# Optimization experiments

Measured on AMD Instinct MI355X. Metric: run time of the kernel, lower is better.

The kernel has to match this reference:

```python
import jax, jax.numpy as jnp
import numpy as np

N, E, D_IN, D_OUT = 50000, 800000, 128, 64


def setup_inputs() -> dict:
    key = jax.random.key(0)
    ks = jax.random.split(key, 8)
    s = 1.0 / np.sqrt(D_IN)
    return {
        "x": jax.random.normal(ks[0], (N, D_IN), jnp.float32),
        "edge_index": jax.random.randint(ks[1], (2, E), 0, N),
        "edge_weight": jax.random.uniform(ks[2], (E,), jnp.float32),
        "init_w": jax.random.normal(ks[3], (D_IN, D_IN), jnp.float32) * s,
        "gru_w_ih": jax.random.normal(ks[4], (3 * D_IN, D_IN), jnp.float32) * s,
        "gru_w_hh": jax.random.normal(ks[5], (3 * D_IN, D_IN), jnp.float32) * s,
        "gru_b_ih": jnp.zeros((3 * D_IN,), jnp.float32),
        "gru_b_hh": jnp.zeros((3 * D_IN,), jnp.float32),
        "lin_w": jax.random.normal(ks[6], (D_OUT, D_IN), jnp.float32) * s,
        "lin_b": jnp.zeros((D_OUT,), jnp.float32),
    }


def _gru_step(x, h, w_ih, w_hh, b_ih, b_hh):
    # torch GRU gate order: r, z, n
    gi = x @ w_ih.T + b_ih
    gh = h @ w_hh.T + b_hh
    i_r, i_z, i_n = jnp.split(gi, 3, axis=-1)
    h_r, h_z, h_n = jnp.split(gh, 3, axis=-1)
    r = jax.nn.sigmoid(i_r + h_r)
    z = jax.nn.sigmoid(i_z + h_z)
    n = jnp.tanh(i_n + r * h_n)
    return (1.0 - z) * n + z * h


def reference(x, edge_index, edge_weight, init_w, gru_w_ih, gru_w_hh, gru_b_ih, gru_b_hh, lin_w, lin_b):
    n_nodes = x.shape[0]
    # EvolveGCNO: evolve W via one GRU step, W is both input and hidden (rows = GRU batch)
    W = _gru_step(init_w, init_w, gru_w_ih, gru_w_hh, gru_b_ih, gru_b_hh)  # [D_IN, D_IN]

    # gcn_norm with self-loops (fill value 1.0)
    loop = jnp.arange(n_nodes)
    row = jnp.concatenate([edge_index[0], loop])  # source j
    col = jnp.concatenate([edge_index[1], loop])  # target i
    w = jnp.concatenate([edge_weight, jnp.ones((n_nodes,), x.dtype)])
    deg = jax.ops.segment_sum(w, col, num_segments=n_nodes)
    dis = jnp.where(deg > 0, jax.lax.rsqrt(jnp.maximum(deg, 1e-12)), 0.0)
    norm = dis[row] * w * dis[col]  # [E+N]

    xw = x @ W  # [N, D_IN]
    h = jax.ops.segment_sum(norm[:, None] * xw[row], col, num_segments=n_nodes)
    h = jax.nn.relu(h)
    return h @ lin_w.T + lin_b  # [N, D_OUT]
```

## Files before the change

### kernel.cpp

```cpp
#include <hip/hip_runtime.h>
#include <hip/hip_fp16.h>
#include <math.h>

#define NN 50000
#define NE 800000
#define D  128
#define D3 384
#define DO 64

typedef _Float16 f16x2 __attribute__((ext_vector_type(2)));

__device__ __forceinline__ float dot2acc(unsigned int h2bits, unsigned int wbits,
                                         float acc) {
#if __has_builtin(__builtin_amdgcn_fdot2)
  return __builtin_amdgcn_fdot2(__builtin_bit_cast(f16x2, h2bits),
                                __builtin_bit_cast(f16x2, wbits), acc, false);
#else
  float2 hf = __half22float2(__builtin_bit_cast(__half2, h2bits));
  float2 wf = __half22float2(__builtin_bit_cast(__half2, wbits));
  return acc + hf.x * wf.x + hf.y * wf.y;
#endif
}

__device__ __forceinline__ unsigned int pk_f16(float a, float b) {
#if __has_builtin(__builtin_amdgcn_cvt_pkrtz)
  return __builtin_bit_cast(unsigned int, __builtin_amdgcn_cvt_pkrtz(a, b));
#else
  return __builtin_bit_cast(unsigned int, __floats2half2_rn(a, b));
#endif
}

__global__ __launch_bounds__(256) void setup_kernel(
    const float* __restrict__ init_w, const float* __restrict__ w_ih,
    const float* __restrict__ w_hh, const float* __restrict__ b_ih,
    const float* __restrict__ b_hh, __half* __restrict__ Wh,
    unsigned long long* __restrict__ packed, int* __restrict__ total) {
  if (blockIdx.x >= 64) {
    int i = (blockIdx.x - 64) * 256 + threadIdx.x;
    if (i < NN) packed[i] = (1ULL << 32);
    if (i == 0) *total = 0;
    return;
  }
  int idx = blockIdx.x * 256 + threadIdx.x;
  int b = idx >> 7;
  int j = idx & 127;
  const float* xr = init_w + b * D;
  const float* wr_i = w_ih + j * D;
  const float* wz_i = w_ih + (D + j) * D;
  const float* wn_i = w_ih + (2 * D + j) * D;
  const float* wr_h = w_hh + j * D;
  const float* wz_h = w_hh + (D + j) * D;
  const float* wn_h = w_hh + (2 * D + j) * D;
  float ir = 0.f, iz = 0.f, in_ = 0.f, hr = 0.f, hz = 0.f, hn = 0.f;
#pragma unroll 4
  for (int k = 0; k < D; ++k) {
    float xv = xr[k];
    ir += xv * wr_i[k];
    iz += xv * wz_i[k];
    in_ += xv * wn_i[k];
    hr += xv * wr_h[k];
    hz += xv * wz_h[k];
    hn += xv * wn_h[k];
  }
  ir += b_ih[j];       hr += b_hh[j];
  iz += b_ih[D + j];   hz += b_hh[D + j];
  in_ += b_ih[2 * D + j]; hn += b_hh[2 * D + j];
  float r = 1.f / (1.f + expf(-(ir + hr)));
  float z = 1.f / (1.f + expf(-(iz + hz)));
  float n = tanhf(in_ + r * hn);
  Wh[idx] = (__half)((1.f - z) * n + z * init_w[idx]);
}

__global__ __launch_bounds__(256) void count_deg_kernel(const int* __restrict__ col,
                                                        const float* __restrict__ ew,
                                                        unsigned long long* __restrict__ packed,
                                                        int* __restrict__ rank) {
  int e = blockIdx.x * 256 + threadIdx.x;
  if (e < NE) {
    int c = __builtin_nontemporal_load(&col[e]);
    float w = __builtin_nontemporal_load(&ew[e]);
    unsigned long long add = (1ULL << 40) | (unsigned long long)(w * 4294967296.0f);
    unsigned long long old = atomicAdd(&packed[c], add);
    __builtin_nontemporal_store((int)(old >> 40), &rank[e]);
  }
}

__global__ __launch_bounds__(256) void dis_scan_kernel(
    const unsigned long long* __restrict__ packed, float* __restrict__ dis,
    int* __restrict__ cnt, int* __restrict__ start, int* __restrict__ total) {
  int i = blockIdx.x * 256 + threadIdx.x;
  int lane = threadIdx.x & 63;
  int c = 0;
  float d = 1.0f;
  if (i < NN) {
    unsigned long long p = packed[i];
    c = (int)(p >> 40);
    d = (float)(p & ((1ULL << 40) - 1)) * 0x1p-32f;
  }
  int cp = (c + 3) & ~3;
  int pre = cp;
#pragma unroll
  for (int off = 1; off < 64; off <<= 1) {
    int t = __shfl_up(pre, off, 64);
    if (lane >= off) pre += t;
  }
  int excl = pre - cp;
  int wtot = __shfl(pre, 63, 64);
  int base = 0;
  if (lane == 63) base = atomicAdd(total, wtot);
  base = __shfl(base, 63, 64);
  if (i < NN) {
    start[i] = base + excl;
    cnt[i] = c;
    dis[i] = rsqrtf(fmaxf(d, 1e-12f));
  }
}

__global__ __launch_bounds__(256) void bucket_kernel(
    const int* __restrict__ row, const int* __restrict__ col,
    const float* __restrict__ ew, const int* __restrict__ rank,
    const int* __restrict__ start, unsigned int* __restrict__ epack) {
  int e = blockIdx.x * 256 + threadIdx.x;
  if (e >= NE) return;
  int j = __builtin_nontemporal_load(&row[e]);
  int c = __builtin_nontemporal_load(&col[e]);
  float w = __builtin_nontemporal_load(&ew[e]);
  int rk = __builtin_nontemporal_load(&rank[e]);
  unsigned short wb = __builtin_bit_cast(unsigned short, (_Float16)w);
  int slot = start[c] + rk;
  __builtin_nontemporal_store((unsigned int)j | ((unsigned int)wb << 16),
                              &epack[slot]);
}

__global__ __launch_bounds__(256) void xw_kernel(const float* __restrict__ x,
                                                 const __half* __restrict__ Wh,
                                                 const float* __restrict__ dis,
                                                 __half* __restrict__ ywh) {
  __shared__ unsigned int U[64 * 128];
  {
    const unsigned short* Wu = (const unsigned short*)Wh;
    for (int i = threadIdx.x; i < 64 * 128; i += 256) {
      int kp = i >> 7, c = i & 127;
      unsigned int lo = Wu[(2 * kp) * D + c];
      unsigned int hi = Wu[(2 * kp + 1) * D + c];
      U[i] = lo | (hi << 16);
    }
  }
  __syncthreads();
  const int t = threadIdx.x;
  const int rr = t >> 4;
  const int ci = t & 15;
  const uint4* U4 = (const uint4*)U;
  for (int base = blockIdx.x * 32; base < NN; base += gridDim.x * 32) {
    float acc[2][8];
#pragma unroll
    for (int q = 0; q < 2; ++q)
#pragma unroll
      for (int j = 0; j < 8; ++j) acc[q][j] = 0.f;
    const int r0 = base + rr;
    const int r1 = r0 + 16;
    const bool v0 = r0 < NN, v1 = r1 < NN;
    const float* xp0 = x + (long)r0 * D;
    const float* xp1 = x + (long)r1 * D;
#pragma unroll 2
    for (int k0 = 0; k0 < D; k0 += 4) {
      float4 xa = v0 ? *(const float4*)(xp0 + k0) : make_float4(0.f, 0.f, 0.f, 0.f);
      float4 xb = v1 ? *(const float4*)(xp1 + k0) : make_float4(0.f, 0.f, 0.f, 0.f);
      unsigned int xa0 = pk_f16(xa.x, xa.y), xa1 = pk_f16(xa.z, xa.w);
      unsigned int xb0 = pk_f16(xb.x, xb.y), xb1 = pk_f16(xb.z, xb.w);
      int kp = k0 >> 1;
      uint4 wA = U4[kp * 32 + 2 * ci];
      uint4 wB = U4[kp * 32 + 2 * ci + 1];
      uint4 wC = U4[(kp + 1) * 32 + 2 * ci];
      uint4 wD = U4[(kp + 1) * 32 + 2 * ci + 1];
      acc[0][0] = dot2acc(xa0, wA.x, acc[0][0]);
      acc[0][1] = dot2acc(xa0, wA.y, acc[0][1]);
      acc[0][2] = dot2acc(xa0, wA.z, acc[0][2]);
      acc[0][3] = dot2acc(xa0, wA.w, acc[0][3]);
      acc[0][4] = dot2acc(xa0, wB.x, acc[0][4]);
      acc[0][5] = dot2acc(xa0, wB.y, acc[0][5]);
      acc[0][6] = dot2acc(xa0, wB.z, acc[0][6]);
      acc[0][7] = dot2acc(xa0, wB.w, acc[0][7]);
      acc[1][0] = dot2acc(xb0, wA.x, acc[1][0]);
      acc[1][1] = dot2acc(xb0, wA.y, acc[1][1]);
      acc[1][2] = dot2acc(xb0, wA.z, acc[1][2]);
      acc[1][3] = dot2acc(xb0, wA.w, acc[1][3]);
      acc[1][4] = dot2acc(xb0, wB.x, acc[1][4]);
      acc[1][5] = dot2acc(xb0, wB.y, acc[1][5]);
      acc[1][6] = dot2acc(xb0, wB.z, acc[1][6]);
      acc[1][7] = dot2acc(xb0, wB.w, acc[1][7]);
      acc[0][0] = dot2acc(xa1, wC.x, acc[0][0]);
      acc[0][1] = dot2acc(xa1, wC.y, acc[0][1]);
      acc[0][2] = dot2acc(xa1, wC.z, acc[0][2]);
      acc[0][3] = dot2acc(xa1, wC.w, acc[0][3]);
      acc[0][4] = dot2acc(xa1, wD.x, acc[0][4]);
      acc[0][5] = dot2acc(xa1, wD.y, acc[0][5]);
      acc[0][6] = dot2acc(xa1, wD.z, acc[0][6]);
      acc[0][7] = dot2acc(xa1, wD.w, acc[0][7]);
      acc[1][0] = dot2acc(xb1, wC.x, acc[1][0]);
      acc[1][1] = dot2acc(xb1, wC.y, acc[1][1]);
      acc[1][2] = dot2acc(xb1, wC.z, acc[1][2]);
      acc[1][3] = dot2acc(xb1, wC.w, acc[1][3]);
      acc[1][4] = dot2acc(xb1, wD.x, acc[1][4]);
      acc[1][5] = dot2acc(xb1, wD.y, acc[1][5]);
      acc[1][6] = dot2acc(xb1, wD.z, acc[1][6]);
      acc[1][7] = dot2acc(xb1, wD.w, acc[1][7]);
    }
#pragma unroll
    for (int q = 0; q < 2; ++q) {
      int r = r0 + q * 16;
      if (r < NN) {
        float ds = dis[r];
        unsigned int pk[4];
#pragma unroll
        for (int j = 0; j < 4; ++j)
          pk[j] = __builtin_bit_cast(unsigned int,
                                     __floats2half2_rn(ds * acc[q][2 * j],
                                                       ds * acc[q][2 * j + 1]));
        *(uint4*)(ywh + (long)r * D + ci * 8) = *(uint4*)pk;
      }
    }
  }
}

__global__ __launch_bounds__(256) void gather_out_kernel(
    const int* __restrict__ start, const int* __restrict__ cnt,
    const unsigned int* __restrict__ epack, const float* __restrict__ dis,
    const __half* __restrict__ ywh, const float* __restrict__ lin_w,
    const float* __restrict__ lin_b, float* __restrict__ out) {
  __shared__ unsigned int LTh[64 * 64];
  __shared__ unsigned int hb[4][2][64];
  for (int idx = threadIdx.x; idx < 64 * 64; idx += 256) {
    int kk = idx >> 6, o = idx & 63;
    __half2 w2 = __floats2half2_rn(lin_w[o * D + 2 * kk], lin_w[o * D + 2 * kk + 1]);
    LTh[idx] = __builtin_bit_cast(unsigned int, w2);
  }
  __syncthreads();
  const int wv = threadIdx.x >> 6;
  const int lane = threadIdx.x & 63;
  const float bias = lin_b[lane];
  const __half2* __restrict__ yw2 = (const __half2*)ywh;
  int gw = blockIdx.x * 4 + wv;
  int nw = gridDim.x * 4;
  for (int i = gw; i < NN; i += 2 * nw) {
    const int iB = i + nw;
    const bool hasB = iB < NN;
    float2 svA = __half22float2(yw2[(long)i * 64 + lane]);
    float aA0 = svA.x, aA1 = svA.y;
    float aB0 = 0.f, aB1 = 0.f;
    int sA = start[i], seA = sA + cnt[i];
    int sB = 0, seB = 0;
    if (hasB) {
      float2 svB = __half22float2(yw2[(long)iB * 64 + lane]);
      aB0 = svB.x;
      aB1 = svB.y;
      sB = start[iB];
      seB = sB + cnt[iB];
    }
    while (sA + 4 <= seA && sB + 4 <= seB) {
      uint4 pA = *(const uint4*)(epack + sA);
      uint4 pB = *(const uint4*)(epack + sB);
      __half2 vA0 = yw2[(long)(pA.x & 0xffff) * 64 + lane];
      __half2 vA1 = yw2[(long)(pA.y & 0xffff) * 64 + lane];
      __half2 vA2 = yw2[(long)(pA.z & 0xffff) * 64 + lane];
      __half2 vA3 = yw2[(long)(pA.w & 0xffff) * 64 + lane];
      __half2 vB0 = yw2[(long)(pB.x & 0xffff) * 64 + lane];
      __half2 vB1 = yw2[(long)(pB.y & 0xffff) * 64 + lane];
      __half2 vB2 = yw2[(long)(pB.z & 0xffff) * 64 + lane];
      __half2 vB3 = yw2[(long)(pB.w & 0xffff) * 64 + lane];
      _Float16 wA0 = __builtin_bit_cast(_Float16, (unsigned short)(pA.x >> 16));
      _Float16 wA1 = __builtin_bit_cast(_Float16, (unsigned short)(pA.y >> 16));
      _Float16 wA2 = __builtin_bit_cast(_Float16, (unsigned short)(pA.z >> 16));
      _Float16 wA3 = __builtin_bit_cast(_Float16, (unsigned short)(pA.w >> 16));
      _Float16 wB0 = __builtin_bit_cast(_Float16, (unsigned short)(pB.x >> 16));
      _Float16 wB1 = __builtin_bit_cast(_Float16, (unsigned short)(pB.y >> 16));
      _Float16 wB2 = __builtin_bit_cast(_Float16, (unsigned short)(pB.z >> 16));
      _Float16 wB3 = __builtin_bit_cast(_Float16, (unsigned short)(pB.w >> 16));
      aA0 += (float)wA0 * (float)__low2half(vA0) + (float)wA1 * (float)__low2half(vA1) +
             (float)wA2 * (float)__low2half(vA2) + (float)wA3 * (float)__low2half(vA3);
      aA1 += (float)wA0 * (float)__high2half(vA0) + (float)wA1 * (float)__high2half(vA1) +
             (float)wA2 * (float)__high2half(vA2) + (float)wA3 * (float)__high2half(vA3);
      aB0 += (float)wB0 * (float)__low2half(vB0) + (float)wB1 * (float)__low2half(vB1) +
             (float)wB2 * (float)__low2half(vB2) + (float)wB3 * (float)__low2half(vB3);
      aB1 += (float)wB0 * (float)__high2half(vB0) + (float)wB1 * (float)__high2half(vB1) +
             (float)wB2 * (float)__high2half(vB2) + (float)wB3 * (float)__high2half(vB3);
      sA += 4;
      sB += 4;
    }
    for (; sA + 4 <= seA; sA += 4) {
      uint4 p = *(const uint4*)(epack + sA);
      __half2 v0 = yw2[(long)(p.x & 0xffff) * 64 + lane];
      __half2 v1 = yw2[(long)(p.y & 0xffff) * 64 + lane];
      __half2 v2 = yw2[(long)(p.z & 0xffff) * 64 + lane];
      __half2 v3 = yw2[(long)(p.w & 0xffff) * 64 + lane];
      _Float16 w0 = __builtin_bit_cast(_Float16, (unsigned short)(p.x >> 16));
      _Float16 w1 = __builtin_bit_cast(_Float16, (unsigned short)(p.y >> 16));
      _Float16 w2 = __builtin_bit_cast(_Float16, (unsigned short)(p.z >> 16));
      _Float16 w3 = __builtin_bit_cast(_Float16, (unsigned short)(p.w >> 16));
      aA0 += (float)w0 * (float)__low2half(v0) + (float)w1 * (float)__low2half(v1) +
             (float)w2 * (float)__low2half(v2) + (float)w3 * (float)__low2half(v3);
      aA1 += (float)w0 * (float)__high2half(v0) + (float)w1 * (float)__high2half(v1) +
             (float)w2 * (float)__high2half(v2) + (float)w3 * (float)__high2half(v3);
    }
    for (; sA < seA; ++sA) {
      unsigned int p = epack[sA];
      _Float16 w0 = __builtin_bit_cast(_Float16, (unsigned short)(p >> 16));
      __half2 v0 = yw2[(long)(p & 0xffff) * 64 + lane];
      aA0 += (float)w0 * (float)__low2half(v0);
      aA1 += (float)w0 * (float)__high2half(v0);
    }
    for (; sB + 4 <= seB; sB += 4) {
      uint4 p = *(const uint4*)(epack + sB);
      __half2 v0 = yw2[(long)(p.x & 0xffff) * 64 + lane];
      __half2 v1 = yw2[(long)(p.y & 0xffff) * 64 + lane];
      __half2 v2 = yw2[(long)(p.z & 0xffff) * 64 + lane];
      __half2 v3 = yw2[(long)(p.w & 0xffff) * 64 + lane];
      _Float16 w0 = __builtin_bit_cast(_Float16, (unsigned short)(p.x >> 16));
      _Float16 w1 = __builtin_bit_cast(_Float16, (unsigned short)(p.y >> 16));
      _Float16 w2 = __builtin_bit_cast(_Float16, (unsigned short)(p.z >> 16));
      _Float16 w3 = __builtin_bit_cast(_Float16, (unsigned short)(p.w >> 16));
      aB0 += (float)w0 * (float)__low2half(v0) + (float)w1 * (float)__low2half(v1) +
             (float)w2 * (float)__low2half(v2) + (float)w3 * (float)__low2half(v3);
      aB1 += (float)w0 * (float)__high2half(v0) + (float)w1 * (float)__high2half(v1) +
             (float)w2 * (float)__high2half(v2) + (float)w3 * (float)__high2half(v3);
    }
    for (; sB < seB; ++sB) {
      unsigned int p = epack[sB];
      _Float16 w0 = __builtin_bit_cast(_Float16, (unsigned short)(p >> 16));
      __half2 v0 = yw2[(long)(p & 0xffff) * 64 + lane];
      aB0 += (float)w0 * (float)__low2half(v0);
      aB1 += (float)w0 * (float)__high2half(v0);
    }
    float dsA = dis[i];
    hb[wv][0][lane] = __builtin_bit_cast(
        unsigned int, __floats2half2_rn(fmaxf(dsA * aA0, 0.f), fmaxf(dsA * aA1, 0.f)));
    if (hasB) {
      float dsB = dis[iB];
      hb[wv][1][lane] = __builtin_bit_cast(
          unsigned int, __floats2half2_rn(fmaxf(dsB * aB0, 0.f), fmaxf(dsB * aB1, 0.f)));
    }
    asm volatile("s_waitcnt lgkmcnt(0)" ::: "memory");
    {
      float ac0 = bias, ac1 = 0.f, ac2 = 0.f, ac3 = 0.f;
      const uint4* hrow = (const uint4*)&hb[wv][0][0];
#pragma unroll
      for (int c = 0; c < 16; ++c) {
        uint4 v = hrow[c];
        ac0 = dot2acc(v.x, LTh[(4 * c + 0) * 64 + lane], ac0);
        ac1 = dot2acc(v.y, LTh[(4 * c + 1) * 64 + lane], ac1);
        ac2 = dot2acc(v.z, LTh[(4 * c + 2) * 64 + lane], ac2);
        ac3 = dot2acc(v.w, LTh[(4 * c + 3) * 64 + lane], ac3);
      }
      __builtin_nontemporal_store((ac0 + ac1) + (ac2 + ac3),
                                  &out[(long)i * DO + lane]);
    }
    if (hasB) {
      float ac0 = bias, ac1 = 0.f, ac2 = 0.f, ac3 = 0.f;
      const uint4* hrow = (const uint4*)&hb[wv][1][0];
#pragma unroll
      for (int c = 0; c < 16; ++c) {
        uint4 v = hrow[c];
        ac0 = dot2acc(v.x, LTh[(4 * c + 0) * 64 + lane], ac0);
        ac1 = dot2acc(v.y, LTh[(4 * c + 1) * 64 + lane], ac1);
        ac2 = dot2acc(v.z, LTh[(4 * c + 2) * 64 + lane], ac2);
        ac3 = dot2acc(v.w, LTh[(4 * c + 3) * 64 + lane], ac3);
      }
      __builtin_nontemporal_store((ac0 + ac1) + (ac2 + ac3),
                                  &out[(long)iB * DO + lane]);
    }
    asm volatile("s_waitcnt lgkmcnt(0)" ::: "memory");
  }
}

extern "C" void kernel_launch(void* const* d_in, const int* in_sizes, int n_in,
                              void* d_out, int out_size, void* d_ws, size_t ws_size,
                              hipStream_t stream) {
  const float* x      = (const float*)d_in[0];
  const int*   eidx   = (const int*)d_in[1];
  const float* ew     = (const float*)d_in[2];
  const float* init_w = (const float*)d_in[3];
  const float* w_ih   = (const float*)d_in[4];
  const float* w_hh   = (const float*)d_in[5];
  const float* b_ih   = (const float*)d_in[6];
  const float* b_hh   = (const float*)d_in[7];
  const float* lin_w  = (const float*)d_in[8];
  const float* lin_b  = (const float*)d_in[9];
  float* out = (float*)d_out;
  const int* row = eidx;
  const int* col = eidx + NE;

  float* ws    = (float*)d_ws;
  __half* Wh   = (__half*)ws;
  unsigned long long* packed = (unsigned long long*)(ws + 8192);
  float* dis   = (float*)(packed + 50048);
  int*   cnt   = (int*)(dis + 50048);
  int*   strt  = cnt + 50048;
  int*   total = strt + 50048;
  int*   rank  = total + 64;
  unsigned int* epack = (unsigned int*)(rank + NE);
  __half* ywh  = (__half*)(epack + 1000064);

  setup_kernel<<<64 + (NN + 255) / 256, 256, 0, stream>>>(init_w, w_ih, w_hh, b_ih,
                                                          b_hh, Wh, packed, total);
  count_deg_kernel<<<(NE + 255) / 256, 256, 0, stream>>>(col, ew, packed, rank);
  dis_scan_kernel<<<(NN + 255) / 256, 256, 0, stream>>>(packed, dis, cnt, strt, total);
  bucket_kernel<<<(NE + 255) / 256, 256, 0, stream>>>(row, col, ew, rank, strt, epack);
  xw_kernel<<<1563, 256, 0, stream>>>(x, Wh, dis, ywh);
  gather_out_kernel<<<2048, 256, 0, stream>>>(strt, cnt, epack, dis, ywh,
                                              lin_w, lin_b, out);
}
```

Baseline: 187.6 us.

## Fuse degree counting with XW GEMM and fold edge norms into bucketed edges

Degree counting and the x@W product now run in one launch, with separate block ranges doing each job, so the atomic-bound edge pass can overlap the GEMM. Because xw no longer depends on dis, the full normalisation dis[j]*w*dis[c] is computed once per edge in the bucket pass and stored as the fp16 weight. The self-loop term becomes dis^2 times xw. The gather kernel now processes four nodes per wave instead of two to expose more memory-level parallelism. The trade-off is extra random dis lookups in the bucket kernel, normalised weights rounded to fp16, and more register pressure in the gather.

```diff
diff --git a/kernel.cpp b/kernel.cpp
--- a/kernel.cpp
+++ b/kernel.cpp
@@ -7,6 +7,9 @@
 #define D  128
 #define D3 384
 #define DO 64
+
+#define CD_BLOCKS 3125
+#define XW_BLOCKS 1563
 
 typedef _Float16 f16x2 __attribute__((ext_vector_type(2)));
 
@@ -71,72 +74,23 @@
   Wh[idx] = (__half)((1.f - z) * n + z * init_w[idx]);
 }
 
-__global__ __launch_bounds__(256) void count_deg_kernel(const int* __restrict__ col,
-                                                        const float* __restrict__ ew,
-                                                        unsigned long long* __restrict__ packed,
-                                                        int* __restrict__ rank) {
-  int e = blockIdx.x * 256 + threadIdx.x;
-  if (e < NE) {
-    int c = __builtin_nontemporal_load(&col[e]);
-    float w = __builtin_nontemporal_load(&ew[e]);
-    unsigned long long add = (1ULL << 40) | (unsigned long long)(w * 4294967296.0f);
-    unsigned long long old = atomicAdd(&packed[c], add);
-    __builtin_nontemporal_store((int)(old >> 40), &rank[e]);
-  }
-}
-
-__global__ __launch_bounds__(256) void dis_scan_kernel(
-    const unsigned long long* __restrict__ packed, float* __restrict__ dis,
-    int* __restrict__ cnt, int* __restrict__ start, int* __restrict__ total) {
-  int i = blockIdx.x * 256 + threadIdx.x;
-  int lane = threadIdx.x & 63;
-  int c = 0;
-  float d = 1.0f;
-  if (i < NN) {
-    unsigned long long p = packed[i];
-    c = (int)(p >> 40);
-    d = (float)(p & ((1ULL << 40) - 1)) * 0x1p-32f;
-  }
-  int cp = (c + 3) & ~3;
-  int pre = cp;
-#pragma unroll
-  for (int off = 1; off < 64; off <<= 1) {
-    int t = __shfl_up(pre, off, 64);
-    if (lane >= off) pre += t;
-  }
-  int excl = pre - cp;
-  int wtot = __shfl(pre, 63, 64);
-  int base = 0;
-  if (lane == 63) base = atomicAdd(total, wtot);
-  base = __shfl(base, 63, 64);
-  if (i < NN) {
-    start[i] = base + excl;
-    cnt[i] = c;
-    dis[i] = rsqrtf(fmaxf(d, 1e-12f));
-  }
-}
-
-__global__ __launch_bounds__(256) void bucket_kernel(
-    const int* __restrict__ row, const int* __restrict__ col,
-    const float* __restrict__ ew, const int* __restrict__ rank,
-    const int* __restrict__ start, unsigned int* __restrict__ epack) {
-  int e = blockIdx.x * 256 + threadIdx.x;
-  if (e >= NE) return;
-  int j = __builtin_nontemporal_load(&row[e]);
-  int c = __builtin_nontemporal_load(&col[e]);
-  float w = __builtin_nontemporal_load(&ew[e]);
-  int rk = __builtin_nontemporal_load(&rank[e]);
-  unsigned short wb = __builtin_bit_cast(unsigned short, (_Float16)w);
-  int slot = start[c] + rk;
-  __builtin_nontemporal_store((unsigned int)j | ((unsigned int)wb << 16),
-                              &epack[slot]);
-}
-
-__global__ __launch_bounds__(256) void xw_kernel(const float* __restrict__ x,
-                                                 const __half* __restrict__ Wh,
-                                                 const float* __restrict__ dis,
-                                                 __half* __restrict__ ywh) {
+__global__ __launch_bounds__(256) void xwcd_kernel(
+    const float* __restrict__ x, const __half* __restrict__ Wh,
+    const int* __restrict__ col, const float* __restrict__ ew,
+    unsigned long long* __restrict__ packed, int* __restrict__ rank,
+    __half* __restrict__ xwh) {
   __shared__ unsigned int U[64 * 128];
+  if (blockIdx.x < CD_BLOCKS) {
+    int e = blockIdx.x * 256 + threadIdx.x;
+    if (e < NE) {
+      int c = __builtin_nontemporal_load(&col[e]);
+      float w = __builtin_nontemporal_load(&ew[e]);
+      unsigned long long add = (1ULL << 40) | (unsigned long long)(w * 4294967296.0f);
+      unsigned long long old = atomicAdd(&packed[c], add);
+      __builtin_nontemporal_store((int)(old >> 40), &rank[e]);
+    }
+    return;
+  }
   {
     const unsigned short* Wu = (const unsigned short*)Wh;
     for (int i = threadIdx.x; i < 64 * 128; i += 256) {
@@ -151,7 +105,8 @@
   const int rr = t >> 4;
   const int ci = t & 15;
   const uint4* U4 = (const uint4*)U;
-  for (int base = blockIdx.x * 32; base < NN; base += gridDim.x * 32) {
+  const int xb = blockIdx.x - CD_BLOCKS;
+  for (int base = xb * 32; base < NN; base += XW_BLOCKS * 32) {
     float acc[2][8];
 #pragma unroll
     for (int q = 0; q < 2; ++q)
@@ -165,9 +120,9 @@
 #pragma unroll 2
     for (int k0 = 0; k0 < D; k0 += 4) {
       float4 xa = v0 ? *(const float4*)(xp0 + k0) : make_float4(0.f, 0.f, 0.f, 0.f);
-      float4 xb = v1 ? *(const float4*)(xp1 + k0) : make_float4(0.f, 0.f, 0.f, 0.f);
+      float4 xb4 = v1 ? *(const float4*)(xp1 + k0) : make_float4(0.f, 0.f, 0.f, 0.f);
       unsigned int xa0 = pk_f16(xa.x, xa.y), xa1 = pk_f16(xa.z, xa.w);
-      unsigned int xb0 = pk_f16(xb.x, xb.y), xb1 = pk_f16(xb.z, xb.w);
+      unsigned int xb0 = pk_f16(xb4.x, xb4.y), xb1 = pk_f16(xb4.z, xb4.w);
       int kp = k0 >> 1;
       uint4 wA = U4[kp * 32 + 2 * ci];
       uint4 wB = U4[kp * 32 + 2 * ci + 1];
@@ -210,26 +165,101 @@
     for (int q = 0; q < 2; ++q) {
       int r = r0 + q * 16;
       if (r < NN) {
-        float ds = dis[r];
         unsigned int pk[4];
 #pragma unroll
         for (int j = 0; j < 4; ++j)
-          pk[j] = __builtin_bit_cast(unsigned int,
-                                     __floats2half2_rn(ds * acc[q][2 * j],
-                                                       ds * acc[q][2 * j + 1]));
-        *(uint4*)(ywh + (long)r * D + ci * 8) = *(uint4*)pk;
+          pk[j] = __builtin_bit_cast(
+              unsigned int, __floats2half2_rn(acc[q][2 * j], acc[q][2 * j + 1]));
+        *(uint4*)(xwh + (long)r * D + ci * 8) = *(uint4*)pk;
       }
     }
   }
 }
+
+__global__ __launch_bounds__(256) void dis_scan_kernel(
+    const unsigned long long* __restrict__ packed, float* __restrict__ dis,
+    int* __restrict__ cnt, int* __restrict__ start, int* __restrict__ total) {
+  int i = blockIdx.x * 256 + threadIdx.x;
+  int lane = threadIdx.x & 63;
+  int c = 0;
+  float d = 1.0f;
+  if (i < NN) {
+    unsigned long long p = packed[i];
+    c = (int)(p >> 40);
+    d = (float)(p & ((1ULL << 40) - 1)) * 0x1p-32f;
+  }
+  int cp = (c + 3) & ~3;
+  int pre = cp;
+#pragma unroll
+  for (int off = 1; off < 64; off <<= 1) {
+    int t = __shfl_up(pre, off, 64);
+    if (lane >= off) pre += t;
+  }
+  int excl = pre - cp;
+  int wtot = __shfl(pre, 63, 64);
+  int base = 0;
+  if (lane == 63) base = atomicAdd(total, wtot);
+  base = __shfl(base, 63, 64);
+  if (i < NN) {
+    start[i] = base + excl;
+    cnt[i] = c;
+    dis[i] = rsqrtf(fmaxf(d, 1e-12f));
+  }
+}
+
+__global__ __launch_bounds__(256) void bucket_kernel(
+    const int* __restrict__ row, const int* __restrict__ col,
+    const float* __restrict__ ew, const int* __restrict__ rank,
+    const float* __restrict__ dis, const int* __restrict__ start,
+    unsigned int* __restrict__ epack) {
+  int e = blockIdx.x * 256 + threadIdx.x;
+  if (e >= NE) return;
+  int j = __builtin_nontemporal_load(&row[e]);
+  int c = __builtin_nontemporal_load(&col[e]);
+  float w = __builtin_nontemporal_load(&ew[e]);
+  int rk = __builtin_nontemporal_load(&rank[e]);
+  float nrm = dis[j] * w * dis[c];
+  unsigned short wb = __builtin_bit_cast(unsigned short, (_Float16)nrm);
+  int slot = start[c] + rk;
+  __builtin_nontemporal_store((unsigned int)j | ((unsigned int)wb << 16),
+                              &epack[slot]);
+}
+
+#define EDGE4(p_, a0_, a1_)                                                     \
+  {                                                                             \
+    __half2 v0_ = yw2[(long)(p_.x & 0xffff) * 64 + lane];                       \
+    __half2 v1_ = yw2[(long)(p_.y & 0xffff) * 64 + lane];                       \
+    __half2 v2_ = yw2[(long)(p_.z & 0xffff) * 64 + lane];                       \
+    __half2 v3_ = yw2[(long)(p_.w & 0xffff) * 64 + lane];                       \
+    _Float16 w0_ = __builtin_bit_cast(_Float16, (unsigned short)(p_.x >> 16));  \
+    _Float16 w1_ = __builtin_bit_cast(_Float16, (unsigned short)(p_.y >> 16));  \
+    _Float16 w2_ = __builtin_bit_cast(_Float16, (unsigned short)(p_.z >> 16));  \
+    _Float16 w3_ = __builtin_bit_cast(_Float16, (unsigned short)(p_.w >> 16));  \
+    a0_ += (float)w0_ * (float)__low2half(v0_) +                                \
+           (float)w1_ * (float)__low2half(v1_) +                                \
+           (float)w2_ * (float)__low2half(v2_) +                                \
+           (float)w3_ * (float)__low2half(v3_);                                 \
+    a1_ += (float)w0_ * (float)__high2half(v0_) +                               \
+           (float)w1_ * (float)__high2half(v1_) +                               \
+           (float)w2_ * (float)__high2half(v2_) +                               \
+           (float)w3_ * (float)__high2half(v3_);                                \
+  }
+#define EDGE1(s_, a0_, a1_)                                                     \
+  {                                                                             \
+    unsigned int p_ = epack[s_];                                                \
+    _Float16 w0_ = __builtin_bit_cast(_Float16, (unsigned short)(p_ >> 16));    \
+    __half2 v0_ = yw2[(long)(p_ & 0xffff) * 64 + lane];                         \
+    a0_ += (float)w0_ * (float)__low2half(v0_);                                 \
+    a1_ += (float)w0_ * (float)__high2half(v0_);                                \
+  }
 
 __global__ __launch_bounds__(256) void gather_out_kernel(
     const int* __restrict__ start, const int* __restrict__ cnt,
     const unsigned int* __restrict__ epack, const float* __restrict__ dis,
-    const __half* __restrict__ ywh, const float* __restrict__ lin_w,
+    const __half* __restrict__ xwh, const float* __restrict__ lin_w,
     const float* __restrict__ lin_b, float* __restrict__ out) {
   __shared__ unsigned int LTh[64 * 64];
-  __shared__ unsigned int hb[4][2][64];
+  __shared__ unsigned int hb[4][4][64];
   for (int idx = threadIdx.x; idx < 64 * 64; idx += 256) {
     int kk = idx >> 6, o = idx & 63;
     __half2 w2 = __floats2half2_rn(lin_w[o * D + 2 * kk], lin_w[o * D + 2 * kk + 1]);
@@ -239,134 +269,125 @@
   const int wv = threadIdx.x >> 6;
   const int lane = threadIdx.x & 63;
   const float bias = lin_b[lane];
-  const __half2* __restrict__ yw2 = (const __half2*)ywh;
+  const __half2* __restrict__ yw2 = (const __half2*)xwh;
   int gw = blockIdx.x * 4 + wv;
   int nw = gridDim.x * 4;
-  for (int i = gw; i < NN; i += 2 * nw) {
-    const int iB = i + nw;
-    const bool hasB = iB < NN;
-    float2 svA = __half22float2(yw2[(long)i * 64 + lane]);
-    float aA0 = svA.x, aA1 = svA.y;
-    float aB0 = 0.f, aB1 = 0.f;
-    int sA = start[i], seA = sA + cnt[i];
-    int sB = 0, seB = 0;
+  for (int i = gw; i < NN; i += 4 * nw) {
+    const int iB = i + nw, iC = i + 2 * nw, iD = i + 3 * nw;
+    const bool hasB = iB < NN, hasC = iC < NN, hasD = iD < NN;
+    float aA0, aA1, aB0 = 0.f, aB1 = 0.f, aC0 = 0.f, aC1 = 0.f, aD0 = 0.f, aD1 = 0.f;
+    int sA, seA, sB = 0, seB = 0, sC = 0, seC = 0, sD = 0, seD = 0;
+    {
+      float ds = dis[i], ds2 = ds * ds;
+      float2 sv = __half22float2(yw2[(long)i * 64 + lane]);
+      aA0 = ds2 * sv.x;
+      aA1 = ds2 * sv.y;
+      sA = start[i];
+      seA = sA + cnt[i];
+    }
     if (hasB) {
-      float2 svB = __half22float2(yw2[(long)iB * 64 + lane]);
-      aB0 = svB.x;
-      aB1 = svB.y;
+      float ds = dis[iB], ds2 = ds * ds;
+      float2 sv = __half22float2(yw2[(long)iB * 64 + lane]);
+      aB0 = ds2 * sv.x;
+      aB1 = ds2 * sv.y;
       sB = start[iB];
       seB = sB + cnt[iB];
+    }
+    if (hasC) {
+      float ds = dis[iC], ds2 = ds * ds;
+      float2 sv = __half22float2(yw2[(long)iC * 64 + lane]);
+      aC0 = ds2 * sv.x;
+      aC1 = ds2 * sv.y;
+      sC = start[iC];
+      seC = sC + cnt[iC];
+    }
+    if (hasD) {
+      float ds = dis[iD], ds2 = ds * ds;
+      float2 sv = __half22float2(yw2[(long)iD * 64 + lane]);
+      aD0 = ds2 * sv.x;
+      aD1 = ds2 * sv.y;
+      sD = start[iD];
+      seD = sD + cnt[iD];
+    }
+    while (sA + 4 <= seA && sB + 4 <= seB && sC + 4 <= seC && sD + 4 <= seD) {
+      uint4 pA = *(const uint4*)(epack + sA);
+      uint4 pB = *(const uint4*)(epack + sB);
+      uint4 pC = *(const uint4*)(epack + sC);
+      uint4 pD = *(const uint4*)(epack + sD);
+      EDGE4(pA, aA0, aA1);
+      EDGE4(pB, aB0, aB1);
+      EDGE4(pC, aC0, aC1);
+      EDGE4(pD, aD0, aD1);
+      sA += 4;
+      sB += 4;
+      sC += 4;
+      sD += 4;
     }
     while (sA + 4 <= seA && sB + 4 <= seB) {
       uint4 pA = *(const uint4*)(epack + sA);
       uint4 pB = *(const uint4*)(epack + sB);
-      __half2 vA0 = yw2[(long)(pA.x & 0xffff) * 64 + lane];
-      __half2 vA1 = yw2[(long)(pA.y & 0xffff) * 64 + lane];
-      __half2 vA2 = yw2[(long)(pA.z & 0xffff) * 64 + lane];
-      __half2 vA3 = yw2[(long)(pA.w & 0xffff) * 64 + lane];
-      __half2 vB0 = yw2[(long)(pB.x & 0xffff) * 64 + lane];
-      __half2 vB1 = yw2[(long)(pB.y & 0xffff) * 64 + lane];
-      __half2 vB2 = yw2[(long)(pB.z & 0xffff) * 64 + lane];
-      __half2 vB3 = yw2[(long)(pB.w & 0xffff) * 64 + lane];
-      _Float16 wA0 = __builtin_bit_cast(_Float16, (unsigned short)(pA.x >> 16));
-      _Float16 wA1 = __builtin_bit_cast(_Float16, (unsigned short)(pA.y >> 16));
-      _Float16 wA2 = __builtin_bit_cast(_Float16, (unsigned short)(pA.z >> 16));
-      _Float16 wA3 = __builtin_bit_cast(_Float16, (unsigned short)(pA.w >> 16));
-      _Float16 wB0 = __builtin_bit_cast(_Float16, (unsigned short)(pB.x >> 16));
-      _Float16 wB1 = __builtin_bit_cast(_Float16, (unsigned short)(pB.y >> 16));
-      _Float16 wB2 = __builtin_bit_cast(_Float16, (unsigned short)(pB.z >> 16));
-      _Float16 wB3 = __builtin_bit_cast(_Float16, (unsigned short)(pB.w >> 16));
-      aA0 += (float)wA0 * (float)__low2half(vA0) + (float)wA1 * (float)__low2half(vA1) +
-             (float)wA2 * (float)__low2half(vA2) + (float)wA3 * (float)__low2half(vA3);
-      aA1 += (float)wA0 * (float)__high2half(vA0) + (float)wA1 * (float)__high2half(vA1) +
-             (float)wA2 * (float)__high2half(vA2) + (float)wA3 * (float)__high2half(vA3);
-      aB0 += (float)wB0 * (float)__low2half(vB0) + (float)wB1 * (float)__low2half(vB1) +
-             (float)wB2 * (float)__low2half(vB2) + (float)wB3 * (float)__low2half(vB3);
-      aB1 += (float)wB0 * (float)__high2half(vB0) + (float)wB1 * (float)__high2half(vB1) +
-             (float)wB2 * (float)__high2half(vB2) + (float)wB3 * (float)__high2half(vB3);
+      EDGE4(pA, aA0, aA1);
+      EDGE4(pB, aB0, aB1);
       sA += 4;
       sB += 4;
     }
+    while (sC + 4 <= seC && sD + 4 <= seD) {
+      uint4 pC = *(const uint4*)(epack + sC);
+      uint4 pD = *(const uint4*)(epack + sD);
+      EDGE4(pC, aC0, aC1);
+      EDGE4(pD, aD0, aD1);
+      sC += 4;
+      sD += 4;
+    }
     for (; sA + 4 <= seA; sA += 4) {
       uint4 p = *(const uint4*)(epack + sA);
-      __half2 v0 = yw2[(long)(p.x & 0xffff) * 64 + lane];
-      __half2 v1 = yw2[(long)(p.y & 0xffff) * 64 + lane];
-      __half2 v2 = yw2[(long)(p.z & 0xffff) * 64 + lane];
-      __half2 v3 = yw2[(long)(p.w & 0xffff) * 64 + lane];
-      _Float16 w0 = __builtin_bit_cast(_Float16, (unsigned short)(p.x >> 16));
-      _Float16 w1 = __builtin_bit_cast(_Float16, (unsigned short)(p.y >> 16));
-      _Float16 w2 = __builtin_bit_cast(_Float16, (unsigned short)(p.z >> 16));
-      _Float16 w3 = __builtin_bit_cast(_Float16, (unsigned short)(p.w >> 16));
-      aA0 += (float)w0 * (float)__low2half(v0) + (float)w1 * (float)__low2half(v1) +
-             (float)w2 * (float)__low2half(v2) + (float)w3 * (float)__low2half(v3);
-      aA1 += (float)w0 * (float)__high2half(v0) + (float)w1 * (float)__high2half(v1) +
-             (float)w2 * (float)__high2half(v2) + (float)w3 * (float)__high2half(v3);
-    }
-    for (; sA < seA; ++sA) {
-      unsigned int p = epack[sA];
-      _Float16 w0 = __builtin_bit_cast(_Float16, (unsigned short)(p >> 16));
-      __half2 v0 = yw2[(long)(p & 0xffff) * 64 + lane];
-      aA0 += (float)w0 * (float)__low2half(v0);
-      aA1 += (float)w0 * (float)__high2half(v0);
-    }
+      EDGE4(p, aA0, aA1);
+    }
+    for (; sA < seA; ++sA) EDGE1(sA, aA0, aA1);
     for (; sB + 4 <= seB; sB += 4) {
       uint4 p = *(const uint4*)(epack + sB);
-      __half2 v0 = yw2[(long)(p.x & 0xffff) * 64 + lane];
-      __half2 v1 = yw2[(long)(p.y & 0xffff) * 64 + lane];
-      __half2 v2 = yw2[(long)(p.z & 0xffff) * 64 + lane];
-      __half2 v3 = yw2[(long)(p.w & 0xffff) * 64 + lane];
-      _Float16 w0 = __builtin_bit_cast(_Float16, (unsigned short)(p.x >> 16));
-      _Float16 w1 = __builtin_bit_cast(_Float16, (unsigned short)(p.y >> 16));
-      _Float16 w2 = __builtin_bit_cast(_Float16, (unsigned short)(p.z >> 16));
-      _Float16 w3 = __builtin_bit_cast(_Float16, (unsigned short)(p.w >> 16));
-      aB0 += (float)w0 * (float)__low2half(v0) + (float)w1 * (float)__low2half(v1) +
-             (float)w2 * (float)__low2half(v2) + (float)w3 * (float)__low2half(v3);
-      aB1 += (float)w0 * (float)__high2half(v0) + (float)w1 * (float)__high2half(v1) +
-             (float)w2 * (float)__high2half(v2) + (float)w3 * (float)__high2half(v3);
-    }
-    for (; sB < seB; ++sB) {
-      unsigned int p = epack[sB];
-      _Float16 w0 = __builtin_bit_cast(_Float16, (unsigned short)(p >> 16));
-      __half2 v0 = yw2[(long)(p & 0xffff) * 64 + lane];
-      aB0 += (float)w0 * (float)__low2half(v0);
-      aB1 += (float)w0 * (float)__high2half(v0);
-    }
-    float dsA = dis[i];
+      EDGE4(p, aB0, aB1);
+    }
+    for (; sB < seB; ++sB) EDGE1(sB, aB0, aB1);
+    for (; sC + 4 <= seC; sC += 4) {
+      uint4 p = *(const uint4*)(epack + sC);
+      EDGE4(p, aC0, aC1);
+    }
+    for (; sC < seC; ++sC) EDGE1(sC, aC0, aC1);
+    for (; sD + 4 <= seD; sD += 4) {
+      uint4 p = *(const uint4*)(epack + sD);
+      EDGE4(p, aD0, aD1);
+    }
+    for (; sD < seD; ++sD) EDGE1(sD, aD0, aD1);
     hb[wv][0][lane] = __builtin_bit_cast(
-        unsigned int, __floats2half2_rn(fmaxf(dsA * aA0, 0.f), fmaxf(dsA * aA1, 0.f)));
-    if (hasB) {
-      float dsB = dis[iB];
+        unsigned int, __floats2half2_rn(fmaxf(aA0, 0.f), fmaxf(aA1, 0.f)));
+    if (hasB)
       hb[wv][1][lane] = __builtin_bit_cast(
-          unsigned int, __floats2half2_rn(fmaxf(dsB * aB0, 0.f), fmaxf(dsB * aB1, 0.f)));
-    }
+          unsigned int, __floats2half2_rn(fmaxf(aB0, 0.f), fmaxf(aB1, 0.f)));
+    if (hasC)
+      hb[wv][2][lane] = __builtin_bit_cast(
+          unsigned int, __floats2half2_rn(fmaxf(aC0, 0.f), fmaxf(aC1, 0.f)));
+    if (hasD)
+      hb[wv][3][lane] = __builtin_bit_cast(
+          unsigned int, __floats2half2_rn(fmaxf(aD0, 0.f), fmaxf(aD1, 0.f)));
     asm volatile("s_waitcnt lgkmcnt(0)" ::: "memory");
-    {
-      float ac0 = bias, ac1 = 0.f, ac2 = 0.f, ac3 = 0.f;
-      const uint4* hrow = (const uint4*)&hb[wv][0][0];
-#pragma unroll
-      for (int c = 0; c < 16; ++c) {
-        uint4 v = hrow[c];
-        ac0 = dot2acc(v.x, LTh[(4 * c + 0) * 64 + lane], ac0);
-        ac1 = dot2acc(v.y, LTh[(4 * c + 1) * 64 + lane], ac1);
-        ac2 = dot2acc(v.z, LTh[(4 * c + 2) * 64 + lane], ac2);
-        ac3 = dot2acc(v.w, LTh[(4 * c + 3) * 64 + lane], ac3);
+#pragma unroll
+    for (int q = 0; q < 4; ++q) {
+      int iq = i + q * nw;
+      if (iq < NN) {
+        float ac0 = bias, ac1 = 0.f, ac2 = 0.f, ac3 = 0.f;
+        const uint4* hrow = (const uint4*)&hb[wv][q][0];
+#pragma unroll
+        for (int c = 0; c < 16; ++c) {
+          uint4 v = hrow[c];
+          ac0 = dot2acc(v.x, LTh[(4 * c + 0) * 64 + lane], ac0);
+          ac1 = dot2acc(v.y, LTh[(4 * c + 1) * 64 + lane], ac1);
+          ac2 = dot2acc(v.z, LTh[(4 * c + 2) * 64 + lane], ac2);
+          ac3 = dot2acc(v.w, LTh[(4 * c + 3) * 64 + lane], ac3);
+        }
+        __builtin_nontemporal_store((ac0 + ac1) + (ac2 + ac3),
+                                    &out[(long)iq * DO + lane]);
       }
-      __builtin_nontemporal_store((ac0 + ac1) + (ac2 + ac3),
-                                  &out[(long)i * DO + lane]);
-    }
-    if (hasB) {
-      float ac0 = bias, ac1 = 0.f, ac2 = 0.f, ac3 = 0.f;
-      const uint4* hrow = (const uint4*)&hb[wv][1][0];
-#pragma unroll
-      for (int c = 0; c < 16; ++c) {
-        uint4 v = hrow[c];
-        ac0 = dot2acc(v.x, LTh[(4 * c + 0) * 64 + lane], ac0);
-        ac1 = dot2acc(v.y, LTh[(4 * c + 1) * 64 + lane], ac1);
-        ac2 = dot2acc(v.z, LTh[(4 * c + 2) * 64 + lane], ac2);
-        ac3 = dot2acc(v.w, LTh[(4 * c + 3) * 64 + lane], ac3);
-      }
-      __builtin_nontemporal_store((ac0 + ac1) + (ac2 + ac3),
-                                  &out[(long)iB * DO + lane]);
     }
     asm volatile("s_waitcnt lgkmcnt(0)" ::: "memory");
   }
@@ -398,14 +419,15 @@
   int*   total = strt + 50048;
   int*   rank  = total + 64;
   unsigned int* epack = (unsigned int*)(rank + NE);
-  __half* ywh  = (__half*)(epack + 1000064);
+  __half* xwh  = (__half*)(epack + 1000064);
 
   setup_kernel<<<64 + (NN + 255) / 256, 256, 0, stream>>>(init_w, w_ih, w_hh, b_ih,
                                                           b_hh, Wh, packed, total);
-  count_deg_kernel<<<(NE + 255) / 256, 256, 0, stream>>>(col, ew, packed, rank);
+  xwcd_kernel<<<CD_BLOCKS + XW_BLOCKS, 256, 0, stream>>>(x, Wh, col, ew, packed,
+                                                         rank, xwh);
   dis_scan_kernel<<<(NN + 255) / 256, 256, 0, stream>>>(packed, dis, cnt, strt, total);
-  bucket_kernel<<<(NE + 255) / 256, 256, 0, stream>>>(row, col, ew, rank, strt, epack);
-  xw_kernel<<<1563, 256, 0, stream>>>(x, Wh, dis, ywh);
-  gather_out_kernel<<<2048, 256, 0, stream>>>(strt, cnt, epack, dis, ywh,
+  bucket_kernel<<<(NE + 255) / 256, 256, 0, stream>>>(row, col, ew, rank, dis, strt,
+                                                      epack);
+  gather_out_kernel<<<2048, 256, 0, stream>>>(strt, cnt, epack, dis, xwh,
                                               lin_w, lin_b, out);
 }
```

Result: slower. 205.1 us (+9.3%).

## Fold full edge norm into bucketed weights and drop dis scaling from xw

Applied to the files above, without the earlier changes.

The bucket kernel now stores the full per-edge normalisation dis[j]*w*dis[c] as the fp16 weight, instead of only the raw weight. Because of that, xw no longer needs dis or a scale per row, and the gather uses dis[i]^2 only for the self-loop term. The shared-memory layout of the weight tile in xw is also reordered so each thread reads contiguous uint4 slots at ci and ci+16 rather than 2*ci, aiming to reduce LDS bank conflicts. The trade-off is extra random dis[j] loads in bucket_kernel and slightly different fp16 rounding, since the product is now stored in half precision.

```diff
diff --git a/kernel.cpp b/kernel.cpp
--- a/kernel.cpp
+++ b/kernel.cpp
@@ -119,14 +119,16 @@
 __global__ __launch_bounds__(256) void bucket_kernel(
     const int* __restrict__ row, const int* __restrict__ col,
     const float* __restrict__ ew, const int* __restrict__ rank,
-    const int* __restrict__ start, unsigned int* __restrict__ epack) {
+    const float* __restrict__ dis, const int* __restrict__ start,
+    unsigned int* __restrict__ epack) {
   int e = blockIdx.x * 256 + threadIdx.x;
   if (e >= NE) return;
   int j = __builtin_nontemporal_load(&row[e]);
   int c = __builtin_nontemporal_load(&col[e]);
   float w = __builtin_nontemporal_load(&ew[e]);
   int rk = __builtin_nontemporal_load(&rank[e]);
-  unsigned short wb = __builtin_bit_cast(unsigned short, (_Float16)w);
+  float nrm = dis[j] * w * dis[c];
+  unsigned short wb = __builtin_bit_cast(unsigned short, (_Float16)nrm);
   int slot = start[c] + rk;
   __builtin_nontemporal_store((unsigned int)j | ((unsigned int)wb << 16),
                               &epack[slot]);
@@ -134,8 +136,7 @@
 
 __global__ __launch_bounds__(256) void xw_kernel(const float* __restrict__ x,
                                                  const __half* __restrict__ Wh,
-                                                 const float* __restrict__ dis,
-                                                 __half* __restrict__ ywh) {
+                                                 __half* __restrict__ xwh) {
   __shared__ unsigned int U[64 * 128];
   {
     const unsigned short* Wu = (const unsigned short*)Wh;
@@ -143,7 +144,8 @@
       int kp = i >> 7, c = i & 127;
       unsigned int lo = Wu[(2 * kp) * D + c];
       unsigned int hi = Wu[(2 * kp + 1) * D + c];
-      U[i] = lo | (hi << 16);
+      int sl = (c >> 3) + ((c & 4) ? 16 : 0);
+      U[kp * 128 + sl * 4 + (c & 3)] = lo | (hi << 16);
     }
   }
   __syncthreads();
@@ -169,10 +171,10 @@
       unsigned int xa0 = pk_f16(xa.x, xa.y), xa1 = pk_f16(xa.z, xa.w);
       unsigned int xb0 = pk_f16(xb.x, xb.y), xb1 = pk_f16(xb.z, xb.w);
       int kp = k0 >> 1;
-      uint4 wA = U4[kp * 32 + 2 * ci];
-      uint4 wB = U4[kp * 32 + 2 * ci + 1];
-      uint4 wC = U4[(kp + 1) * 32 + 2 * ci];
-      uint4 wD = U4[(kp + 1) * 32 + 2 * ci + 1];
+      uint4 wA = U4[kp * 32 + ci];
+      uint4 wB = U4[kp * 32 + ci + 16];
+      uint4 wC = U4[(kp + 1) * 32 + ci];
+      uint4 wD = U4[(kp + 1) * 32 + ci + 16];
       acc[0][0] = dot2acc(xa0, wA.x, acc[0][0]);
       acc[0][1] = dot2acc(xa0, wA.y, acc[0][1]);
       acc[0][2] = dot2acc(xa0, wA.z, acc[0][2]);
@@ -210,14 +212,12 @@
     for (int q = 0; q < 2; ++q) {
       int r = r0 + q * 16;
       if (r < NN) {
-        float ds = dis[r];
         unsigned int pk[4];
 #pragma unroll
         for (int j = 0; j < 4; ++j)
-          pk[j] = __builtin_bit_cast(unsigned int,
-                                     __floats2half2_rn(ds * acc[q][2 * j],
-                                                       ds * acc[q][2 * j + 1]));
-        *(uint4*)(ywh + (long)r * D + ci * 8) = *(uint4*)pk;
+          pk[j] = __builtin_bit_cast(
+              unsigned int, __floats2half2_rn(acc[q][2 * j], acc[q][2 * j + 1]));
+        *(uint4*)(xwh + (long)r * D + ci * 8) = *(uint4*)pk;
       }
     }
   }
@@ -226,7 +226,7 @@
 __global__ __launch_bounds__(256) void gather_out_kernel(
     const int* __restrict__ start, const int* __restrict__ cnt,
     const unsigned int* __restrict__ epack, const float* __restrict__ dis,
-    const __half* __restrict__ ywh, const float* __restrict__ lin_w,
+    const __half* __restrict__ xwh, const float* __restrict__ lin_w,
     const float* __restrict__ lin_b, float* __restrict__ out) {
   __shared__ unsigned int LTh[64 * 64];
   __shared__ unsigned int hb[4][2][64];
@@ -239,21 +239,23 @@
   const int wv = threadIdx.x >> 6;
   const int lane = threadIdx.x & 63;
   const float bias = lin_b[lane];
-  const __half2* __restrict__ yw2 = (const __half2*)ywh;
+  const __half2* __restrict__ yw2 = (const __half2*)xwh;
   int gw = blockIdx.x * 4 + wv;
   int nw = gridDim.x * 4;
   for (int i = gw; i < NN; i += 2 * nw) {
     const int iB = i + nw;
     const bool hasB = iB < NN;
+    float dsA = dis[i], dsA2 = dsA * dsA;
     float2 svA = __half22float2(yw2[(long)i * 64 + lane]);
-    float aA0 = svA.x, aA1 = svA.y;
+    float aA0 = dsA2 * svA.x, aA1 = dsA2 * svA.y;
     float aB0 = 0.f, aB1 = 0.f;
     int sA = start[i], seA = sA + cnt[i];
     int sB = 0, seB = 0;
     if (hasB) {
+      float dsB = dis[iB], dsB2 = dsB * dsB;
       float2 svB = __half22float2(yw2[(long)iB * 64 + lane]);
-      aB0 = svB.x;
-      aB1 = svB.y;
+      aB0 = dsB2 * svB.x;
+      aB1 = dsB2 * svB.y;
       sB = start[iB];
       seB = sB + cnt[iB];
     }
@@ -331,13 +333,11 @@
       aB0 += (float)w0 * (float)__low2half(v0);
       aB1 += (float)w0 * (float)__high2half(v0);
     }
-    float dsA = dis[i];
     hb[wv][0][lane] = __builtin_bit_cast(
-        unsigned int, __floats2half2_rn(fmaxf(dsA * aA0, 0.f), fmaxf(dsA * aA1, 0.f)));
+        unsigned int, __floats2half2_rn(fmaxf(aA0, 0.f), fmaxf(aA1, 0.f)));
     if (hasB) {
-      float dsB = dis[iB];
       hb[wv][1][lane] = __builtin_bit_cast(
-          unsigned int, __floats2half2_rn(fmaxf(dsB * aB0, 0.f), fmaxf(dsB * aB1, 0.f)));
+          unsigned int, __floats2half2_rn(fmaxf(aB0, 0.f), fmaxf(aB1, 0.f)));
     }
     asm volatile("s_waitcnt lgkmcnt(0)" ::: "memory");
     {
@@ -398,14 +398,15 @@
   int*   total = strt + 50048;
   int*   rank  = total + 64;
   unsigned int* epack = (unsigned int*)(rank + NE);
-  __half* ywh  = (__half*)(epack + 1000064);
+  __half* xwh  = (__half*)(epack + 1000064);
 
   setup_kernel<<<64 + (NN + 255) / 256, 256, 0, stream>>>(init_w, w_ih, w_hh, b_ih,
                                                           b_hh, Wh, packed, total);
   count_deg_kernel<<<(NE + 255) / 256, 256, 0, stream>>>(col, ew, packed, rank);
   dis_scan_kernel<<<(NN + 255) / 256, 256, 0, stream>>>(packed, dis, cnt, strt, total);
-  bucket_kernel<<<(NE + 255) / 256, 256, 0, stream>>>(row, col, ew, rank, strt, epack);
-  xw_kernel<<<1563, 256, 0, stream>>>(x, Wh, dis, ywh);
-  gather_out_kernel<<<2048, 256, 0, stream>>>(strt, cnt, epack, dis, ywh,
+  bucket_kernel<<<(NE + 255) / 256, 256, 0, stream>>>(row, col, ew, rank, dis, strt,
+                                                      epack);
+  xw_kernel<<<1563, 256, 0, stream>>>(x, Wh, xwh);
+  gather_out_kernel<<<2048, 256, 0, stream>>>(strt, cnt, epack, dis, xwh,
                                               lin_w, lin_b, out);
 }
```

Result: no change. 189.4 us (+1.0%).
